# Performance work log

Hardware: AMD Instinct MI355X
Metric: run time of the kernel (lower is better)

## Reference

```python
import jax, jax.numpy as jnp
import numpy as np
from jax import lax

D_MODEL, D_INNER, D_STATE, DT_RANK = 192, 384, 1, 12
B, H, W = 4, 128, 128


def _dwconv_replicate(x, w, dil, pad):
    # x: [B, D, H, W], w: [D, 1, 3, 3]; replicate padding then VALID dilated depthwise conv
    xp = jnp.pad(x, ((0, 0), (0, 0), (pad, pad), (pad, pad)), mode='edge')
    return lax.conv_general_dilated(xp, w, (1, 1), 'VALID', rhs_dilation=(dil, dil),
                                    dimension_numbers=('NCHW', 'OIHW', 'NCHW'),
                                    feature_group_count=x.shape[1])


def setup_inputs() -> dict:
    key = jax.random.key(0)
    ks = jax.random.split(key, 16)
    n = lambda i, shape, s: jax.random.normal(ks[i], shape, dtype=jnp.float32) * s
    return {
        'x': n(0, (B, H, W, D_MODEL), 1.0),
        'Win': n(1, (2 * D_INNER, D_MODEL), D_MODEL ** -0.5),        # in_proj weight (no bias)
        'conv_w': n(2, (D_INNER, 1, 3, 3), 0.3),                      # depthwise conv2d
        'conv_b': n(3, (D_INNER,), 0.1),
        'x_proj_w': n(4, (DT_RANK + 2 * D_STATE, D_INNER), D_INNER ** -0.5),
        'dt_w': n(5, (D_INNER, DT_RANK), DT_RANK ** -0.5),
        'dt_b': n(6, (D_INNER,), 0.1) - 4.0,                          # small softplus(dt)
        'A_logs': jnp.zeros((D_INNER, D_STATE), dtype=jnp.float32),   # log(arange(1,2)) = 0 -> A = -1
        'Ds': jnp.ones((D_INNER,), dtype=jnp.float32),
        'k3': n(7, (D_INNER, 1, 3, 3), 0.2),
        'k3_1': n(8, (D_INNER, 1, 3, 3), 0.2),
        'k3_2': n(9, (D_INNER, 1, 3, 3), 0.2),
        'alpha': jnp.array([1.0, 0.5, 0.25], dtype=jnp.float32),
        'ln_g': jnp.ones((D_INNER,), dtype=jnp.float32),
        'ln_b': jnp.zeros((D_INNER,), dtype=jnp.float32),
        'Wout': n(10, (D_MODEL, D_INNER), D_INNER ** -0.5),
    }


def reference(x, Win, conv_w, conv_b, x_proj_w, dt_w, dt_b, A_logs, Ds,
              k3, k3_1, k3_2, alpha, ln_g, ln_b, Wout):
    Bb, Hh, Ww, _ = x.shape
    L = Hh * Ww
    # in_proj, split x / z
    xz = jnp.einsum('bhwc,ec->bhwe', x, Win)
    xi, z = jnp.split(xz, 2, axis=-1)
    # depthwise conv2d (zero pad 1) + SiLU
    xc = jnp.transpose(xi, (0, 3, 1, 2))  # [B, D, H, W]
    xc = lax.conv_general_dilated(xc, conv_w, (1, 1), ((1, 1), (1, 1)),
                                  dimension_numbers=('NCHW', 'OIHW', 'NCHW'),
                                  feature_group_count=D_INNER) + conv_b[None, :, None, None]
    xc = jax.nn.silu(xc)
    xs = xc.reshape(Bb, D_INNER, L)
    # projections
    x_dbl = jnp.einsum('kd,bdl->bkl', x_proj_w, xs)
    dts = x_dbl[:, :DT_RANK]
    Bs = x_dbl[:, DT_RANK:DT_RANK + D_STATE]          # [B, N, L]
    Cs = x_dbl[:, DT_RANK + D_STATE:]                 # [B, N, L]
    delta = jax.nn.softplus(jnp.einsum('dr,brl->bdl', dt_w, dts) + dt_b[None, :, None])
    A = -jnp.exp(A_logs)                              # [D, N]
    # discretize: dA [B, D, L, N], dBu [B, D, L, N]
    dA = jnp.exp(delta[:, :, :, None] * A[None, :, None, :])
    dBu = delta[:, :, :, None] * jnp.swapaxes(Bs, 1, 2)[:, None, :, :] * xs[:, :, :, None]
    # sequential selective scan over L
    def step(h, t):
        dA_t, dBu_t = t
        h = dA_t * h + dBu_t
        return h, h
    _, hs = lax.scan(step, jnp.zeros((Bb, D_INNER, D_STATE), dtype=x.dtype),
                     (jnp.moveaxis(dA, 2, 0), jnp.moveaxis(dBu, 2, 0)))
    # hs: [L, B, D, N=1] -> spatial state map [B, D, H, W]
    h_map = jnp.moveaxis(hs[..., 0], 0, 2).reshape(Bb, D_INNER, Hh, Ww)
    # StateFusion: multi-dilation depthwise convs with replicate padding
    h1 = _dwconv_replicate(h_map, k3, 1, 1)
    h2 = _dwconv_replicate(h_map, k3_1, 3, 3)
    h3 = _dwconv_replicate(h_map, k3_2, 5, 5)
    h_f = alpha[0] * h1 + alpha[1] * h2 + alpha[2] * h3
    hflat = h_f.reshape(Bb, D_INNER, L)
    y = hflat * Cs + xs * Ds[None, :, None]           # Cs: [B, 1, L] broadcasts over D
    y = jnp.transpose(y.reshape(Bb, D_INNER, Hh, Ww), (0, 2, 3, 1))  # [B, H, W, D]
    # LayerNorm over channels
    mu = jnp.mean(y, axis=-1, keepdims=True)
    var = jnp.mean(jnp.square(y - mu), axis=-1, keepdims=True)
    y = (y - mu) * lax.rsqrt(var + 1e-5) * ln_g + ln_b
    # gate + out_proj
    y = y * jax.nn.silu(z)
    return jnp.einsum('bhwd,cd->bhwc', y, Wout)
```

## Files before the change

### kernel.cpp

```cpp
#include <hip/hip_runtime.h>
#include <hip/hip_bf16.h>

#define D_MODEL 192
#define D_INNER 384
#define DT_RANK 12
#define BATCH   4
#define HH      128
#define WW      128
#define LL      (HH*WW)

typedef __hip_bfloat16 bf16;
typedef __attribute__((ext_vector_type(8))) short short8;
typedef __attribute__((ext_vector_type(4))) float f32x4;

__device__ __forceinline__ float b2f(bf16 v) { return __bfloat162float(v); }
__device__ __forceinline__ bf16  f2b(float v) { return __float2bfloat16(v); }
__device__ __forceinline__ unsigned short fbits(float v) {
    union { bf16 h; unsigned short u; } c; c.h = __float2bfloat16(v); return c.u;
}
__device__ __forceinline__ float bits2f(unsigned short u) {
    union { unsigned u32; float f; } c; c.u32 = (unsigned)u << 16; return c.f;
}
__device__ __forceinline__ float fsig(float x) {
    return __builtin_amdgcn_rcpf(1.f + __expf(-x));
}
__device__ __forceinline__ float fsoftplus(float s) {
    return (s > 20.f) ? s : __logf(1.f + __expf(s));
}

__global__ __launch_bounds__(256) void k_cvt(const float* __restrict__ src,
                                             unsigned short* __restrict__ dst) {
    size_t i = ((size_t)blockIdx.x * 256 + threadIdx.x) * 8;
    float4 f0 = *(const float4*)(src + i);
    float4 f1 = *(const float4*)(src + i + 4);
    unsigned short u[8] = {fbits(f0.x), fbits(f0.y), fbits(f0.z), fbits(f0.w),
                           fbits(f1.x), fbits(f1.y), fbits(f1.z), fbits(f1.w)};
    *(int4*)(dst + i) = *(const int4*)u;
}

__global__ __launch_bounds__(256) void k_padw(const float* __restrict__ dt_w,
                                              unsigned short* __restrict__ wp) {
    int i = blockIdx.x * 256 + threadIdx.x;
    int d = i >> 5, r = i & 31;
    float v = (r < 12) ? dt_w[d * 12 + r] : 0.f;
    wp[i] = fbits(v);
}

__global__ __launch_bounds__(256) void k_gemm_xz(const unsigned short* __restrict__ Xb,
                                                 const unsigned short* __restrict__ Wb,
                                                 bf16* __restrict__ xi,
                                                 bf16* __restrict__ z) {
    __shared__ short Al[128][40];
    __shared__ short Bl[128][40];
    int t = threadIdx.x, lane = t & 63, w = t >> 6;
    int wr = w >> 1, wc = w & 1;
    int n0 = blockIdx.x * 128, m0 = blockIdx.y * 128;
    f32x4 acc[4][4];
    f32x4 zv = {0.f, 0.f, 0.f, 0.f};
    #pragma unroll
    for (int i = 0; i < 4; i++)
        #pragma unroll
        for (int j = 0; j < 4; j++) acc[i][j] = zv;

    int sr = t >> 1, sc = (t & 1) * 16;
    const unsigned short* Ab = Xb + (size_t)(m0 + sr) * D_MODEL + sc;
    const unsigned short* Bb = Wb + (size_t)(n0 + sr) * D_MODEL + sc;

    for (int k0 = 0; k0 < D_MODEL; k0 += 32) {
        int4 av0 = *(const int4*)(Ab + k0);
        int4 av1 = *(const int4*)(Ab + k0 + 8);
        int4 bv0 = *(const int4*)(Bb + k0);
        int4 bv1 = *(const int4*)(Bb + k0 + 8);
        __syncthreads();
        *(int4*)&Al[sr][sc]     = av0;
        *(int4*)&Al[sr][sc + 8] = av1;
        *(int4*)&Bl[sr][sc]     = bv0;
        *(int4*)&Bl[sr][sc + 8] = bv1;
        __syncthreads();
        short8 af[4], bfr[4];
        #pragma unroll
        for (int f = 0; f < 4; f++) {
            af[f]  = *(const short8*)&Al[wr * 64 + f * 16 + (lane & 15)][(lane >> 4) * 8];
            bfr[f] = *(const short8*)&Bl[wc * 64 + f * 16 + (lane & 15)][(lane >> 4) * 8];
        }
        #pragma unroll
        for (int i = 0; i < 4; i++)
            #pragma unroll
            for (int j = 0; j < 4; j++)
                acc[i][j] = __builtin_amdgcn_mfma_f32_16x16x32_bf16(af[i], bfr[j], acc[i][j], 0, 0, 0);
    }

    #pragma unroll
    for (int i = 0; i < 4; i++) {
        int mB = m0 + wr * 64 + i * 16 + ((lane >> 4) << 2);
        int lb = mB >> 14, l = mB & (LL - 1);
        #pragma unroll
        for (int j = 0; j < 4; j++) {
            int n = n0 + wc * 64 + j * 16 + (lane & 15);
            f32x4 v = acc[i][j];
            if (n < D_INNER) {
                union { short4 s4; unsigned short u[4]; } p;
                #pragma unroll
                for (int r = 0; r < 4; r++) p.u[r] = fbits(v[r]);
                *(short4*)&xi[((size_t)lb * D_INNER + n) * LL + l] = p.s4;
            } else {
                #pragma unroll
                for (int r = 0; r < 4; r++)
                    z[(size_t)(mB + r) * D_INNER + (n - D_INNER)] = f2b(v[r]);
            }
        }
    }
}

__global__ __launch_bounds__(256) void k_conv_silu(const bf16* __restrict__ xi,
                                                   const float* __restrict__ w,
                                                   const float* __restrict__ bias,
                                                   bf16* __restrict__ xs) {
    __shared__ float rb[18][144];
    int bid = blockIdx.x;
    int dl = bid >> 3;
    int d  = dl % D_INNER;
    int y0 = (bid & 7) * 16;
    int t  = threadIdx.x;
    const bf16* src = xi + (size_t)dl * LL;

    for (int rr = (t >> 4); rr < 18; rr += 16) {
        int c  = t & 15;
        int yy = y0 + rr - 1;
        float vals[8];
        if (yy >= 0 && yy < HH) {
            short8 s8 = *(const short8*)&src[yy * WW + c * 8];
            #pragma unroll
            for (int j = 0; j < 8; j++) vals[j] = bits2f((unsigned short)s8[j]);
        } else {
            #pragma unroll
            for (int j = 0; j < 8; j++) vals[j] = 0.f;
        }
        *(float4*)&rb[rr][8 + c * 8]     = *(float4*)&vals[0];
        *(float4*)&rb[rr][8 + c * 8 + 4] = *(float4*)&vals[4];
        if (c == 0)  rb[rr][7]   = 0.f;
        if (c == 15) rb[rr][136] = 0.f;
    }
    float wk[9];
    #pragma unroll
    for (int k = 0; k < 9; k++) wk[k] = w[d * 9 + k];
    float bs = bias[d];
    __syncthreads();

    int x = t & 127, half = t >> 7;
    int Rb = half * 8;
    float out[8];
    #pragma unroll
    for (int i = 0; i < 8; i++) out[i] = bs;
    #pragma unroll
    for (int dx = 0; dx < 3; dx++) {
        float v[10];
        #pragma unroll
        for (int k = 0; k < 10; k++) v[k] = rb[Rb + k][7 + x + dx];
        #pragma unroll
        for (int i = 0; i < 8; i++)
            out[i] += v[i] * wk[dx] + v[i + 1] * wk[3 + dx] + v[i + 2] * wk[6 + dx];
    }
    #pragma unroll
    for (int i = 0; i < 8; i++) {
        float s = out[i] * fsig(out[i]);
        xs[(size_t)dl * LL + (y0 + Rb + i) * WW + x] = f2b(s);
    }
}

__global__ __launch_bounds__(256) void k_xdbl(const bf16* __restrict__ xs,
                                              const float* __restrict__ xpw,
                                              unsigned short* __restrict__ dtsb,
                                              float* __restrict__ bsd,
                                              float* __restrict__ csd) {
    __shared__ float part[4][64][17];
    int bid = blockIdx.x;
    int lb  = bid >> 8;
    int l0  = (bid & 255) * 64;
    int t = threadIdx.x;
    int l = t & 63, dg = t >> 6;

    const bf16* base = xs + (size_t)lb * D_INNER * LL + l0 + l;
    float acc[14] = {};
    for (int d0 = dg * 96; d0 < dg * 96 + 96; d0 += 8) {
        float v[8];
        #pragma unroll
        for (int q = 0; q < 8; q++) v[q] = b2f(base[(size_t)(d0 + q) * LL]);
        #pragma unroll
        for (int q = 0; q < 8; q++) {
            #pragma unroll
            for (int k = 0; k < 14; k++) acc[k] += xpw[k * D_INNER + d0 + q] * v[q];
        }
    }
    #pragma unroll
    for (int k = 0; k < 14; k++) part[dg][l][k] = acc[k];
    __syncthreads();

    if (t < 64) {
        float s[14];
        #pragma unroll
        for (int k = 0; k < 14; k++)
            s[k] = part[0][t][k] + part[1][t][k] + part[2][t][k] + part[3][t][k];
        unsigned short pk[32];
        #pragma unroll
        for (int k = 0; k < 12; k++) pk[k] = fbits(s[k]);
        #pragma unroll
        for (int k = 12; k < 32; k++) pk[k] = 0;
        int4* dst = (int4*)&dtsb[((size_t)lb * LL + l0 + t) << 5];
        #pragma unroll
        for (int q = 0; q < 4; q++) dst[q] = ((const int4*)pk)[q];
        bsd[(size_t)lb * LL + l0 + t] = s[12];
        csd[(size_t)lb * LL + l0 + t] = s[13];
    }
}

__global__ __launch_bounds__(256) void k_delta(const unsigned short* __restrict__ wp,
                                               const unsigned short* __restrict__ dtsb,
                                               const float* __restrict__ dt_b,
                                               bf16* __restrict__ delta) {
    __shared__ float bsm[16];
    int m0 = blockIdx.x * 16;
    int nbk = blockIdx.y;
    int lb = nbk >> 5;
    int n0 = (nbk & 31) * 512;
    int t = threadIdx.x, lane = t & 63, w = t >> 6;
    if (t < 16) bsm[t] = dt_b[m0 + t];
    short8 af = *(const short8*)&wp[(m0 + (lane & 15)) * 32 + (lane >> 4) * 8];
    __syncthreads();
    f32x4 zv = {0.f, 0.f, 0.f, 0.f};
    int row = (lane >> 4) * 4;
    #pragma unroll
    for (int s = 0; s < 8; s++) {
        int n = n0 + w * 128 + s * 16 + (lane & 15);
        short8 bf8 = *(const short8*)&dtsb[(((size_t)lb * LL + n) << 5) + (lane >> 4) * 8];
        f32x4 c = __builtin_amdgcn_mfma_f32_16x16x32_bf16(af, bf8, zv, 0, 0, 0);
        #pragma unroll
        for (int r = 0; r < 4; r++) {
            float sv = c[r] + bsm[row + r];
            float dl = fsoftplus(sv);
            delta[((size_t)lb * D_INNER + m0 + row + r) * LL + n] = f2b(dl);
        }
    }
}

__global__ __launch_bounds__(512, 4) void k_scan(const bf16* __restrict__ xs,
                                                 const bf16* __restrict__ delta,
                                                 const float* __restrict__ bsd,
                                                 const float* __restrict__ A_logs,
                                                 bf16* __restrict__ h) {
    int seq = blockIdx.x;
    int d   = seq % D_INNER;
    int lb  = seq / D_INNER;
    int t    = threadIdx.x;
    int lane = t & 63;
    int wid  = t >> 6;

    float Aval = -__expf(A_logs[d]);

    int l0 = t * 32;
    const bf16* xv = xs + (size_t)seq * LL + l0;
    const bf16* dv = delta + (size_t)seq * LL + l0;
    const float* bsp = bsd + (size_t)lb * LL + l0;

    float xsv[32], dlv[32];
    {
        int4 raw[4], rawd[4];
        const int4* src = (const int4*)xv;
        const int4* srcd = (const int4*)dv;
        #pragma unroll
        for (int q = 0; q < 4; q++) { raw[q] = src[q]; rawd[q] = srcd[q]; }
        const unsigned short* u = (const unsigned short*)raw;
        const unsigned short* ud = (const unsigned short*)rawd;
        #pragma unroll
        for (int j = 0; j < 32; j++) { xsv[j] = bits2f(u[j]); dlv[j] = bits2f(ud[j]); }
    }

    float a[32], bb[32];
    float Ar = 1.f, Br = 0.f;
    #pragma unroll
    for (int j = 0; j < 32; j++) {
        float Bsv = bsp[j];
        float dl = dlv[j];
        float av = __expf(dl * Aval);
        float bv = dl * Bsv * xsv[j];
        a[j] = av; bb[j] = bv;
        Br = av * Br + bv;
        Ar *= av;
    }

    #pragma unroll
    for (int off = 1; off < 64; off <<= 1) {
        float Ap = __shfl_up(Ar, off);
        float Bp = __shfl_up(Br, off);
        if (lane >= off) { Br = Ar * Bp + Br; Ar *= Ap; }
    }

    __shared__ float LA[8], LB[8];
    if (lane == 63) { LA[wid] = Ar; LB[wid] = Br; }
    __syncthreads();
    float Bwp = 0.f;
    for (int ww = 0; ww < wid; ww++) { Bwp = LA[ww] * Bwp + LB[ww]; }

    float Ae = __shfl_up(Ar, 1), Be = __shfl_up(Br, 1);
    if (lane == 0) { Ae = 1.f; Be = 0.f; }
    float hcur = Ae * Bwp + Be;

    unsigned pk[16];
    unsigned lo = 0;
    #pragma unroll
    for (int j = 0; j < 32; j++) {
        hcur = a[j] * hcur + bb[j];
        unsigned bits = fbits(hcur);
        if (j & 1) pk[j >> 1] = lo | (bits << 16);
        else       lo = bits;
    }
    int4* dst = (int4*)(h + (size_t)seq * LL + l0);
    #pragma unroll
    for (int q = 0; q < 4; q++) dst[q] = ((int4*)pk)[q];
}

__global__ __launch_bounds__(256) void k_mconv(const bf16* __restrict__ h,
                                               const float* __restrict__ k1w,
                                               const float* __restrict__ k2w,
                                               const float* __restrict__ k3w,
                                               const float* __restrict__ alpha,
                                               bf16* __restrict__ hf) {
    __shared__ float rb[26][144];
    int bid = blockIdx.x;
    int dl = bid >> 3;
    int d  = dl % D_INNER;
    int y0 = (bid & 7) * 16;
    int t  = threadIdx.x;
    const bf16* src = h + (size_t)dl * LL;

    for (int rr = (t >> 4); rr < 26; rr += 16) {
        int c  = t & 15;
        int yy = min(max(y0 + rr - 5, 0), HH - 1);
        short8 s8 = *(const short8*)&src[yy * WW + c * 8];
        float vals[8];
        #pragma unroll
        for (int j = 0; j < 8; j++) vals[j] = bits2f((unsigned short)s8[j]);
        *(float4*)&rb[rr][8 + c * 8]     = *(float4*)&vals[0];
        *(float4*)&rb[rr][8 + c * 8 + 4] = *(float4*)&vals[4];
        if (c == 0) {
            #pragma unroll
            for (int q = 3; q < 8; q++) rb[rr][q] = vals[0];
        }
        if (c == 15) {
            #pragma unroll
            for (int q = 0; q < 5; q++) rb[rr][136 + q] = vals[7];
        }
    }
    float a0 = alpha[0], a1 = alpha[1], a2 = alpha[2];
    float w1[9], w2[9], w3[9];
    #pragma unroll
    for (int k = 0; k < 9; k++) {
        w1[k] = a0 * k1w[d * 9 + k];
        w2[k] = a1 * k2w[d * 9 + k];
        w3[k] = a2 * k3w[d * 9 + k];
    }
    __syncthreads();

    int x = t & 127, half = t >> 7;
    int Rb = half * 8;
    float out[8] = {};
    #pragma unroll
    for (int dx = 0; dx < 3; dx++) {
        float v[10];
        #pragma unroll
        for (int k = 0; k < 10; k++) v[k] = rb[Rb + 4 + k][7 + x + dx];
        #pragma unroll
        for (int i = 0; i < 8; i++)
            out[i] += v[i] * w1[dx] + v[i + 1] * w1[3 + dx] + v[i + 2] * w1[6 + dx];
    }
    #pragma unroll
    for (int dx = 0; dx < 3; dx++) {
        float v[14];
        #pragma unroll
        for (int k = 0; k < 14; k++) v[k] = rb[Rb + 2 + k][8 + x + 3 * (dx - 1)];
        #pragma unroll
        for (int i = 0; i < 8; i++)
            out[i] += v[i] * w2[dx] + v[i + 3] * w2[3 + dx] + v[i + 6] * w2[6 + dx];
    }
    #pragma unroll
    for (int dx = 0; dx < 3; dx++) {
        float v[18];
        #pragma unroll
        for (int k = 0; k < 18; k++) v[k] = rb[Rb + k][8 + x + 5 * (dx - 1)];
        #pragma unroll
        for (int i = 0; i < 8; i++)
            out[i] += v[i] * w3[dx] + v[i + 5] * w3[3 + dx] + v[i + 10] * w3[6 + dx];
    }
    #pragma unroll
    for (int i = 0; i < 8; i++)
        hf[(size_t)dl * LL + (y0 + Rb + i) * WW + x] = f2b(out[i]);
}

__global__ __launch_bounds__(256) void k_ln(const bf16* __restrict__ hf,
                                            const bf16* __restrict__ xs,
                                            const float* __restrict__ csd,
                                            const float* __restrict__ Ds,
                                            const float* __restrict__ ln_g,
                                            const float* __restrict__ ln_b,
                                            const bf16* __restrict__ z,
                                            bf16* __restrict__ yout) {
    __shared__ float vt[384][36];
    __shared__ float csh[32], mu[32], rs[32];
    __shared__ float gsh[384], bsh[384], dsh[384];
    __shared__ float sred[8][33], qred[8][33];

    int bid = blockIdx.x;
    int lb = bid >> 9;
    int l0 = (bid & 511) * 32;
    int t = threadIdx.x;

    if (t < 32) csh[t] = csd[(size_t)lb * LL + l0 + t];
    for (int i = t; i < 384; i += 256) {
        gsh[i] = ln_g[i]; bsh[i] = ln_b[i]; dsh[i] = Ds[i];
    }
    __syncthreads();

    #pragma unroll
    for (int p = 0; p < 6; p++) {
        int d = p * 64 + (t >> 2);
        int loff = (t & 3) * 8;
        size_t off = ((size_t)lb * D_INNER + d) * LL + l0 + loff;
        short8 h8 = *(const short8*)&hf[off];
        short8 x8 = *(const short8*)&xs[off];
        float dsv = dsh[d];
        float vv[8];
        #pragma unroll
        for (int j = 0; j < 8; j++)
            vv[j] = bits2f((unsigned short)h8[j]) * csh[loff + j]
                  + bits2f((unsigned short)x8[j]) * dsv;
        *(float4*)&vt[d][loff]     = *(float4*)&vv[0];
        *(float4*)&vt[d][loff + 4] = *(float4*)&vv[4];
    }
    __syncthreads();

    {
        int l = t & 31, ch = t >> 5;
        float s = 0.f, q = 0.f;
        #pragma unroll 8
        for (int dd = 0; dd < 48; dd++) {
            float v = vt[ch * 48 + dd][l];
            s += v; q += v * v;
        }
        sred[ch][l] = s; qred[ch][l] = q;
    }
    __syncthreads();
    if (t < 32) {
        float s = 0.f, q = 0.f;
        #pragma unroll
        for (int c = 0; c < 8; c++) { s += sred[c][t]; q += qred[c][t]; }
        float m = s * (1.f / D_INNER);
        float var = q * (1.f / D_INNER) - m * m;
        mu[t] = m; rs[t] = rsqrtf(var + 1e-5f);
    }
    __syncthreads();

    {
        int l = t & 31, ch = t >> 5;
        int d0 = ch * 48;
        size_t row = ((size_t)lb * LL + l0 + l) * D_INNER + d0;
        const short8* zp = (const short8*)&z[row];
        short8* yp = (short8*)&yout[row];
        float m = mu[l], r = rs[l];
        #pragma unroll
        for (int c = 0; c < 6; c++) {
            short8 z8 = zp[c];
            unsigned short ub[8];
            #pragma unroll
            for (int j = 0; j < 8; j++) {
                int d = d0 + c * 8 + j;
                float v = vt[d][l];
                float yn = (v - m) * r * gsh[d] + bsh[d];
                float zv = bits2f((unsigned short)z8[j]);
                float sz = zv * fsig(zv);
                ub[j] = fbits(yn * sz);
            }
            yp[c] = *(short8*)ub;
        }
    }
}

__global__ __launch_bounds__(256) void k_gemm_out(const bf16* __restrict__ Y,
                                                  const unsigned short* __restrict__ Wb,
                                                  float* __restrict__ out,
                                                  int b_off) {
    __shared__ short Al[128][40];
    __shared__ short Bl[64][40];
    int t = threadIdx.x, lane = t & 63, w = t >> 6;
    int wr = w >> 1, wc = w & 1;
    int n0 = blockIdx.x * 64, m0 = blockIdx.y * 128;
    f32x4 acc[4][2];
    f32x4 zv = {0.f, 0.f, 0.f, 0.f};
    #pragma unroll
    for (int i = 0; i < 4; i++) { acc[i][0] = zv; acc[i][1] = zv; }

    int sr = t >> 1, sc = (t & 1) * 16;
    const unsigned short* Ab = (const unsigned short*)Y + (size_t)(m0 + sr) * D_INNER + sc;
    int br = t >> 2, bc = (t & 3) * 8;
    const unsigned short* Bb = Wb + (size_t)(n0 + br) * D_INNER + bc;

    for (int k0 = 0; k0 < D_INNER; k0 += 32) {
        int4 av0 = *(const int4*)(Ab + k0);
        int4 av1 = *(const int4*)(Ab + k0 + 8);
        int4 bv0 = *(const int4*)(Bb + k0);
        __syncthreads();
        *(int4*)&Al[sr][sc]     = av0;
        *(int4*)&Al[sr][sc + 8] = av1;
        *(int4*)&Bl[br][bc]     = bv0;
        __syncthreads();
        short8 af[4], bfr[2];
        #pragma unroll
        for (int f = 0; f < 4; f++)
            af[f] = *(const short8*)&Al[wr * 64 + f * 16 + (lane & 15)][(lane >> 4) * 8];
        #pragma unroll
        for (int f = 0; f < 2; f++)
            bfr[f] = *(const short8*)&Bl[wc * 32 + f * 16 + (lane & 15)][(lane >> 4) * 8];
        #pragma unroll
        for (int i = 0; i < 4; i++)
            #pragma unroll
            for (int j = 0; j < 2; j++)
                acc[i][j] = __builtin_amdgcn_mfma_f32_16x16x32_bf16(af[i], bfr[j], acc[i][j], 0, 0, 0);
    }

    size_t gm = (size_t)b_off * LL + m0;
    #pragma unroll
    for (int i = 0; i < 4; i++) {
        int mB = wr * 64 + i * 16 + ((lane >> 4) << 2);
        #pragma unroll
        for (int j = 0; j < 2; j++) {
            int n = n0 + wc * 32 + j * 16 + (lane & 15);
            f32x4 v = acc[i][j];
            #pragma unroll
            for (int r = 0; r < 4; r++)
                out[(gm + mB + r) * D_MODEL + n] = v[r];
        }
    }
}

extern "C" void kernel_launch(void* const* d_in, const int* in_sizes, int n_in,
                              void* d_out, int out_size, void* d_ws, size_t ws_size,
                              hipStream_t stream) {
    const float* x        = (const float*)d_in[0];
    const float* Win      = (const float*)d_in[1];
    const float* conv_w   = (const float*)d_in[2];
    const float* conv_b   = (const float*)d_in[3];
    const float* x_proj_w = (const float*)d_in[4];
    const float* dt_w     = (const float*)d_in[5];
    const float* dt_b     = (const float*)d_in[6];
    const float* A_logs   = (const float*)d_in[7];
    const float* Ds       = (const float*)d_in[8];
    const float* k3w      = (const float*)d_in[9];
    const float* k3_1w    = (const float*)d_in[10];
    const float* k3_2w    = (const float*)d_in[11];
    const float* alpha    = (const float*)d_in[12];
    const float* ln_g     = (const float*)d_in[13];
    const float* ln_b     = (const float*)d_in[14];
    const float* Wout     = (const float*)d_in[15];

    unsigned short* Winb  = (unsigned short*)d_ws;
    unsigned short* Woutb = Winb + 2 * D_INNER * D_MODEL;
    unsigned short* wpb   = Woutb + D_MODEL * D_INNER;
    char* pbase = (char*)(wpb + D_INNER * 32);

    const size_t head = (size_t)(2 * D_INNER * D_MODEL + D_MODEL * D_INNER + D_INNER * 32) * 2;
    const size_t per_batch = (size_t)4 * D_INNER * LL * 2
                           + (size_t)2 * LL * 4
                           + (size_t)LL * 32 * 2
                           + (size_t)LL * D_MODEL * 2;
    int nb = (int)((ws_size - head) / per_batch);
    if (nb > BATCH) nb = BATCH;
    if (nb < 1) nb = 1;

    size_t Sb = (size_t)nb * D_INNER * LL;
    bf16* b0 = (bf16*)pbase;
    bf16* b1 = b0 + Sb;
    bf16* b2 = b1 + Sb;
    bf16* b3 = b2 + Sb;
    float* bsd = (float*)(b3 + Sb);
    float* csd = bsd + (size_t)nb * LL;
    unsigned short* dtsb = (unsigned short*)(csd + (size_t)nb * LL);
    unsigned short* Xb = dtsb + (size_t)nb * LL * 32;

    k_cvt <<<(2 * D_INNER * D_MODEL) / 2048, 256, 0, stream>>>(Win, Winb);
    k_cvt <<<(D_MODEL * D_INNER) / 2048, 256, 0, stream>>>(Wout, Woutb);
    k_padw<<<(D_INNER * 32) / 256, 256, 0, stream>>>(dt_w, wpb);

    for (int boff = 0; boff < BATCH; boff += nb) {
        int cur = BATCH - boff < nb ? BATCH - boff : nb;
        k_cvt     <<<(cur * LL * D_MODEL) / 2048, 256, 0, stream>>>(x + (size_t)boff * LL * D_MODEL, Xb);
        k_gemm_xz <<<dim3(6, cur * 128), 256, 0, stream>>>(Xb, Winb, b0, b2);
        k_conv_silu<<<cur * D_INNER * 8, 256, 0, stream>>>(b0, conv_w, conv_b, b1);
        k_xdbl    <<<cur * 256, 256, 0, stream>>>(b1, x_proj_w, dtsb, bsd, csd);
        k_delta   <<<dim3(24, cur * 32), 256, 0, stream>>>(wpb, dtsb, dt_b, b0);
        k_scan    <<<cur * D_INNER, 512, 0, stream>>>(b1, b0, bsd, A_logs, b3);
        k_mconv   <<<cur * D_INNER * 8, 256, 0, stream>>>(b3, k3w, k3_1w, k3_2w, alpha, b0);
        k_ln      <<<cur * 512, 256, 0, stream>>>(b0, b1, csd, Ds, ln_g, ln_b, b2, b3);
        k_gemm_out<<<dim3(3, cur * 128), 256, 0, stream>>>(b3, Woutb, (float*)d_out, boff);
    }
}
```

Before: 326.1 us.

## Fuse dt projection and softplus into scan kernel, drop delta buffer

Removes the separate k_delta MFMA kernel and the padded dt_w conversion, and computes delta = softplus(dt_w·dts + dt_b) inside k_scan from the 12-rank dts rows, which are now stored with 16-element padding instead of 32. This avoids writing and re-reading the full B×D×L bf16 delta tensor and one launch. In exchange each scan thread recomputes a 12-term dot product per element and reads the 32-byte dts rows redundantly across all 384 channels, which puts more ALU work and L2 traffic on the latency-bound scan.

```diff
diff --git a/kernel.cpp b/kernel.cpp
--- a/kernel.cpp
+++ b/kernel.cpp
@@ -36,14 +36,6 @@
     unsigned short u[8] = {fbits(f0.x), fbits(f0.y), fbits(f0.z), fbits(f0.w),
                            fbits(f1.x), fbits(f1.y), fbits(f1.z), fbits(f1.w)};
     *(int4*)(dst + i) = *(const int4*)u;
-}
-
-__global__ __launch_bounds__(256) void k_padw(const float* __restrict__ dt_w,
-                                              unsigned short* __restrict__ wp) {
-    int i = blockIdx.x * 256 + threadIdx.x;
-    int d = i >> 5, r = i & 31;
-    float v = (r < 12) ? dt_w[d * 12 + r] : 0.f;
-    wp[i] = fbits(v);
 }
 
 __global__ __launch_bounds__(256) void k_gemm_xz(const unsigned short* __restrict__ Xb,
@@ -201,50 +193,23 @@
         #pragma unroll
         for (int k = 0; k < 14; k++)
             s[k] = part[0][t][k] + part[1][t][k] + part[2][t][k] + part[3][t][k];
-        unsigned short pk[32];
+        unsigned short pk[16];
         #pragma unroll
         for (int k = 0; k < 12; k++) pk[k] = fbits(s[k]);
         #pragma unroll
-        for (int k = 12; k < 32; k++) pk[k] = 0;
-        int4* dst = (int4*)&dtsb[((size_t)lb * LL + l0 + t) << 5];
-        #pragma unroll
-        for (int q = 0; q < 4; q++) dst[q] = ((const int4*)pk)[q];
+        for (int k = 12; k < 16; k++) pk[k] = 0;
+        int4* dst = (int4*)&dtsb[((size_t)lb * LL + l0 + t) << 4];
+        dst[0] = ((const int4*)pk)[0];
+        dst[1] = ((const int4*)pk)[1];
         bsd[(size_t)lb * LL + l0 + t] = s[12];
         csd[(size_t)lb * LL + l0 + t] = s[13];
     }
 }
 
-__global__ __launch_bounds__(256) void k_delta(const unsigned short* __restrict__ wp,
-                                               const unsigned short* __restrict__ dtsb,
-                                               const float* __restrict__ dt_b,
-                                               bf16* __restrict__ delta) {
-    __shared__ float bsm[16];
-    int m0 = blockIdx.x * 16;
-    int nbk = blockIdx.y;
-    int lb = nbk >> 5;
-    int n0 = (nbk & 31) * 512;
-    int t = threadIdx.x, lane = t & 63, w = t >> 6;
-    if (t < 16) bsm[t] = dt_b[m0 + t];
-    short8 af = *(const short8*)&wp[(m0 + (lane & 15)) * 32 + (lane >> 4) * 8];
-    __syncthreads();
-    f32x4 zv = {0.f, 0.f, 0.f, 0.f};
-    int row = (lane >> 4) * 4;
-    #pragma unroll
-    for (int s = 0; s < 8; s++) {
-        int n = n0 + w * 128 + s * 16 + (lane & 15);
-        short8 bf8 = *(const short8*)&dtsb[(((size_t)lb * LL + n) << 5) + (lane >> 4) * 8];
-        f32x4 c = __builtin_amdgcn_mfma_f32_16x16x32_bf16(af, bf8, zv, 0, 0, 0);
-        #pragma unroll
-        for (int r = 0; r < 4; r++) {
-            float sv = c[r] + bsm[row + r];
-            float dl = fsoftplus(sv);
-            delta[((size_t)lb * D_INNER + m0 + row + r) * LL + n] = f2b(dl);
-        }
-    }
-}
-
 __global__ __launch_bounds__(512, 4) void k_scan(const bf16* __restrict__ xs,
-                                                 const bf16* __restrict__ delta,
+                                                 const unsigned short* __restrict__ dtsb,
+                                                 const float* __restrict__ dt_w,
+                                                 const float* __restrict__ dt_b,
                                                  const float* __restrict__ bsd,
                                                  const float* __restrict__ A_logs,
                                                  bf16* __restrict__ h) {
@@ -256,33 +221,41 @@
     int wid  = t >> 6;
 
     float Aval = -__expf(A_logs[d]);
+    float wreg[12];
+    #pragma unroll
+    for (int r = 0; r < 12; r++) wreg[r] = dt_w[d * 12 + r];
+    float bias = dt_b[d];
 
     int l0 = t * 32;
     const bf16* xv = xs + (size_t)seq * LL + l0;
-    const bf16* dv = delta + (size_t)seq * LL + l0;
+    const unsigned short* dts = dtsb + (((size_t)lb * LL + l0) << 4);
     const float* bsp = bsd + (size_t)lb * LL + l0;
 
-    float xsv[32], dlv[32];
+    float xsv[32];
     {
-        int4 raw[4], rawd[4];
+        int4 raw[4];
         const int4* src = (const int4*)xv;
-        const int4* srcd = (const int4*)dv;
-        #pragma unroll
-        for (int q = 0; q < 4; q++) { raw[q] = src[q]; rawd[q] = srcd[q]; }
+        #pragma unroll
+        for (int q = 0; q < 4; q++) raw[q] = src[q];
         const unsigned short* u = (const unsigned short*)raw;
-        const unsigned short* ud = (const unsigned short*)rawd;
-        #pragma unroll
-        for (int j = 0; j < 32; j++) { xsv[j] = bits2f(u[j]); dlv[j] = bits2f(ud[j]); }
+        #pragma unroll
+        for (int j = 0; j < 32; j++) xsv[j] = bits2f(u[j]);
     }
 
     float a[32], bb[32];
     float Ar = 1.f, Br = 0.f;
     #pragma unroll
     for (int j = 0; j < 32; j++) {
-        float Bsv = bsp[j];
-        float dl = dlv[j];
+        short8 r0 = *(const short8*)&dts[j * 16];
+        short8 r1 = *(const short8*)&dts[j * 16 + 8];
+        float s = bias;
+        #pragma unroll
+        for (int k = 0; k < 8; k++) s += wreg[k] * bits2f((unsigned short)r0[k]);
+        #pragma unroll
+        for (int k = 0; k < 4; k++) s += wreg[8 + k] * bits2f((unsigned short)r1[k]);
+        float dl = fsoftplus(s);
         float av = __expf(dl * Aval);
-        float bv = dl * Bsv * xsv[j];
+        float bv = dl * bsp[j] * xsv[j];
         a[j] = av; bb[j] = bv;
         Br = av * Br + bv;
         Ar *= av;
@@ -563,13 +536,12 @@
 
     unsigned short* Winb  = (unsigned short*)d_ws;
     unsigned short* Woutb = Winb + 2 * D_INNER * D_MODEL;
-    unsigned short* wpb   = Woutb + D_MODEL * D_INNER;
-    char* pbase = (char*)(wpb + D_INNER * 32);
-
-    const size_t head = (size_t)(2 * D_INNER * D_MODEL + D_MODEL * D_INNER + D_INNER * 32) * 2;
+    char* pbase = (char*)(Woutb + D_MODEL * D_INNER);
+
+    const size_t head = (size_t)(2 * D_INNER * D_MODEL + D_MODEL * D_INNER) * 2;
     const size_t per_batch = (size_t)4 * D_INNER * LL * 2
                            + (size_t)2 * LL * 4
-                           + (size_t)LL * 32 * 2
+                           + (size_t)LL * 16 * 2
                            + (size_t)LL * D_MODEL * 2;
     int nb = (int)((ws_size - head) / per_batch);
     if (nb > BATCH) nb = BATCH;
@@ -583,11 +555,10 @@
     float* bsd = (float*)(b3 + Sb);
     float* csd = bsd + (size_t)nb * LL;
     unsigned short* dtsb = (unsigned short*)(csd + (size_t)nb * LL);
-    unsigned short* Xb = dtsb + (size_t)nb * LL * 32;
+    unsigned short* Xb = dtsb + (size_t)nb * LL * 16;
 
     k_cvt <<<(2 * D_INNER * D_MODEL) / 2048, 256, 0, stream>>>(Win, Winb);
     k_cvt <<<(D_MODEL * D_INNER) / 2048, 256, 0, stream>>>(Wout, Woutb);
-    k_padw<<<(D_INNER * 32) / 256, 256, 0, stream>>>(dt_w, wpb);
 
     for (int boff = 0; boff < BATCH; boff += nb) {
         int cur = BATCH - boff < nb ? BATCH - boff : nb;
@@ -595,8 +566,7 @@
         k_gemm_xz <<<dim3(6, cur * 128), 256, 0, stream>>>(Xb, Winb, b0, b2);
         k_conv_silu<<<cur * D_INNER * 8, 256, 0, stream>>>(b0, conv_w, conv_b, b1);
         k_xdbl    <<<cur * 256, 256, 0, stream>>>(b1, x_proj_w, dtsb, bsd, csd);
-        k_delta   <<<dim3(24, cur * 32), 256, 0, stream>>>(wpb, dtsb, dt_b, b0);
-        k_scan    <<<cur * D_INNER, 512, 0, stream>>>(b1, b0, bsd, A_logs, b3);
+        k_scan    <<<cur * D_INNER, 512, 0, stream>>>(b1, dtsb, dt_w, dt_b, bsd, A_logs, b3);
         k_mconv   <<<cur * D_INNER * 8, 256, 0, stream>>>(b3, k3w, k3_1w, k3_2w, alpha, b0);
         k_ln      <<<cur * 512, 256, 0, stream>>>(b0, b1, csd, Ds, ln_g, ln_b, b2, b3);
         k_gemm_out<<<dim3(3, cur * 128), 256, 0, stream>>>(b3, Woutb, (float*)d_out, boff);
```

Result: slower. 621.7 us (+90.7%).
